# Optimization experiments

Hardware: AMD Instinct MI355X
Metric: run time of the kernel (lower is better)

Reference implementation:

```python
import jax, jax.numpy as jnp
import numpy as np

N_WIRES = 4
DIM = 16  # 2**4 state-vector length; wire 0 = most significant bit


def _ry(state, theta, wire):
    """Apply RY(theta) on `wire`. state: (N,16) real; theta: (N,) or scalar."""
    s = jnp.moveaxis(state.reshape(-1, 2, 2, 2, 2), 1 + wire, 1)
    c = jnp.cos(theta * 0.5)
    sn = jnp.sin(theta * 0.5)
    if jnp.ndim(theta):
        c = c.reshape(-1, 1, 1, 1)
        sn = sn.reshape(-1, 1, 1, 1)
    s0, s1 = s[:, 0], s[:, 1]
    out = jnp.stack([c * s0 - sn * s1, sn * s0 + c * s1], axis=1)
    return jnp.moveaxis(out, 1, 1 + wire).reshape(-1, DIM)


def _cx_perm(control, target):
    idx = np.arange(DIM)
    cbit = (idx >> (N_WIRES - 1 - control)) & 1
    return np.where(cbit == 1, idx ^ (1 << (N_WIRES - 1 - target)), idx)

# Pauli-Z expectation signs per wire: (16, 4)
_Z_SIGNS = np.stack(
    [1.0 - 2.0 * ((np.arange(DIM) >> (N_WIRES - 1 - w)) & 1) for w in range(N_WIRES)],
    axis=1,
).astype(np.float32)
_CX01 = _cx_perm(0, 1); _CX12 = _cx_perm(1, 2); _CX23 = _cx_perm(2, 3)
_CX02 = _cx_perm(0, 2); _CX13 = _cx_perm(1, 3)


def _init_state(n, dtype):
    return jnp.zeros((n, DIM), dtype).at[:, 0].set(1.0)  # |0000>


def _encode(angles):
    """Fresh device + RY(angle_w) on each wire. angles: (N,4) -> state (N,16)."""
    state = _init_state(angles.shape[0], angles.dtype)
    for w in range(N_WIRES):
        state = _ry(state, angles[:, w], w)
    return state


def _measure_z(state):
    return (state * state) @ jnp.asarray(_Z_SIGNS, state.dtype)  # (N,4)


def _quanv_features(angles, rl_params):
    """Encoder + fixed 8-op 'random layer' (5 RY + 3 CX) + MeasureAll(Z)."""
    s = _encode(angles)
    s = _ry(s, rl_params[0], 0)
    s = _ry(s, rl_params[1], 1)
    s = s[:, _CX02]
    s = _ry(s, rl_params[2], 2)
    s = _ry(s, rl_params[3], 3)
    s = s[:, _CX13]
    s = _ry(s, rl_params[4], 0)
    s = s[:, _CX23]
    return _measure_z(s)  # (N,4)


def _attn_raw(angles):
    """Encoder + CX(0,1),CX(1,2),CX(2,3), measure Z on wire 0."""
    s = _encode(angles)
    s = s[:, _CX01]
    s = s[:, _CX12]
    s = s[:, _CX23]
    return _measure_z(s)[:, 0]  # (N,)


def setup_inputs() -> dict:
    key = jax.random.key(0)
    k1, k2, k3 = jax.random.split(key, 3)
    B = 4096
    x = jax.random.uniform(k1, (B, 784), dtype=jnp.float32)
    rl_params = jax.random.normal(k2, (5,), dtype=jnp.float32)
    W = jax.random.normal(k3, (10, 784), dtype=jnp.float32) * 0.03
    b = jnp.zeros((10,), jnp.float32)
    return {"x": x, "rl_params": rl_params, "W": W, "b": b}


def reference(x, rl_params, W, b):
    B = x.shape[0]
    img = x.reshape(B, 28, 28)
    # 2x2 patches in row-major order -> (B*196, 4) with order [tl, tr, bl, br]
    angles = img.reshape(B, 14, 2, 14, 2).transpose(0, 1, 3, 2, 4).reshape(B * 196, 4)
    feats = _quanv_features(angles, rl_params).reshape(B, 196, 4)
    raw = _attn_raw(feats.reshape(B * 196, 4)).reshape(B, 196)
    attn = jax.nn.softmax(raw, axis=1)
    weighted = (feats * attn[:, :, None]).reshape(B, 4 * 14 * 14)
    logits = weighted @ W.T + b
    return jax.nn.log_softmax(logits, axis=-1)
```

## Files before the change

### kernel.cpp

```cpp
#include <hip/hip_runtime.h>

#define NTHREADS 256
#define NPATCH 196


__device__ __forceinline__ float dot4(float4 a, float4 b) {
    return a.x * b.x + a.y * b.y + a.z * b.z + a.w * b.w;
}

__global__ __launch_bounds__(NTHREADS) void quanv_fused(
    const float* __restrict__ x, const float* __restrict__ rl,
    const float* __restrict__ W, const float* __restrict__ bias,
    float* __restrict__ out)
{
    __shared__ float xs[4][784];

    const int lane = threadIdx.x & 63;
    const int wave = threadIdx.x >> 6;
    const int img  = blockIdx.x * 4 + wave;

    const float4* __restrict__ xsrc = reinterpret_cast<const float4*>(x + (size_t)img * 784);
    float4* xd = reinterpret_cast<float4*>(xs[wave]);
    #pragma unroll
    for (int r = 0; r < 3; ++r) xd[lane + 64 * r] = xsrc[lane + 64 * r];
    if (lane < 4) xd[192 + lane] = xsrc[192 + lane];
    __syncthreads();

    float srl2, crl2, srl4, crl4;
    __sincosf(rl[2], &srl2, &crl2);
    __sincosf(rl[4], &srl4, &crl4);
    const float rl0 = rl[0], rl1 = rl[1], rl3v = rl[3];

    const float* xw = xs[wave];
    auto patchf = [&](int p, float& f0, float& f1, float& f2, float& f3) {
        const int pi = p / 14;
        const int base = 56 * pi + 2 * (p - pi * 14);
        const float2 top = *reinterpret_cast<const float2*>(&xw[base]);
        const float2 bot = *reinterpret_cast<const float2*>(&xw[base + 28]);
        float sa, ca; __sincosf(top.x + rl0, &sa, &ca);
        float s2, c2; __sincosf(bot.x, &s2, &c2);
        f1 = __cosf(top.y + rl1);
        const float cd = __cosf(bot.y + rl3v);
        f0 = crl4 * ca - srl4 * sa * s2;
        f2 = crl2 * ca * c2 - srl2 * s2;
        f3 = f1 * cd * f2;
    };

    const int p0 = lane, p1 = lane + 64, p2 = lane + 128, p3 = 192 + lane;
    const bool has4 = (lane < 4);

    float f00, f01, f02, f03; patchf(p0, f00, f01, f02, f03);
    float f10, f11, f12, f13; patchf(p1, f10, f11, f12, f13);
    float f20, f21, f22, f23; patchf(p2, f20, f21, f22, f23);
    float f30, f31, f32, f33; patchf(has4 ? p3 : p0, f30, f31, f32, f33);

    const float e0 = __expf(__cosf(f00));
    const float e1 = __expf(__cosf(f10));
    const float e2 = __expf(__cosf(f20));
    const float e3 = has4 ? __expf(__cosf(f30)) : 0.f;

    float sv = e0 + e1 + e2 + e3;
    #pragma unroll
    for (int off = 32; off > 0; off >>= 1) sv += __shfl_xor(sv, off);
    const float inv = 1.0f / sv;

    const float sc0 = e0 * inv, sc1 = e1 * inv, sc2 = e2 * inv, sc3 = e3 * inv;
    const float4 g0 = make_float4(f00 * sc0, f01 * sc0, f02 * sc0, f03 * sc0);
    const float4 g1 = make_float4(f10 * sc1, f11 * sc1, f12 * sc1, f13 * sc1);
    const float4 g2 = make_float4(f20 * sc2, f21 * sc2, f22 * sc2, f23 * sc2);
    const float4 g3 = make_float4(f30 * sc3, f31 * sc3, f32 * sc3, f33 * sc3);

    const float4* __restrict__ W4 = reinterpret_cast<const float4*>(W);
    float acc[10];
    #pragma unroll
    for (int k = 0; k < 10; ++k) {
        acc[k] = dot4(g0, W4[k * NPATCH + p0])
               + dot4(g1, W4[k * NPATCH + p1])
               + dot4(g2, W4[k * NPATCH + p2]);
    }
    if (has4) {
        #pragma unroll
        for (int k = 0; k < 10; ++k) acc[k] += dot4(g3, W4[k * NPATCH + p3]);
    }

    #pragma unroll
    for (int k = 0; k < 10; ++k) {
        #pragma unroll
        for (int off = 32; off > 0; off >>= 1) acc[k] += __shfl_xor(acc[k], off);
        acc[k] += bias[k];
    }

    float m2 = acc[0];
    #pragma unroll
    for (int k = 1; k < 10; ++k) m2 = fmaxf(m2, acc[k]);
    float ssum = 0.f;
    #pragma unroll
    for (int k = 0; k < 10; ++k) ssum += __expf(acc[k] - m2);
    const float lse = m2 + __logf(ssum);

    if (lane < 10) {
        float myv = acc[0];
        #pragma unroll
        for (int k = 1; k < 10; ++k) myv = (lane == k) ? acc[k] : myv;
        out[(size_t)img * 10 + lane] = myv - lse;
    }
}

extern "C" void kernel_launch(void* const* d_in, const int* in_sizes, int n_in,
                              void* d_out, int out_size, void* d_ws, size_t ws_size,
                              hipStream_t stream) {
    const float* x    = (const float*)d_in[0];
    const float* rl   = (const float*)d_in[1];
    const float* W    = (const float*)d_in[2];
    const float* bias = (const float*)d_in[3];
    float* out = (float*)d_out;
    const int B = in_sizes[0] / 784;
    quanv_fused<<<B / 4, NTHREADS, 0, stream>>>(x, rl, W, bias, out);
}
```

Measured before the change: 13.44 us.

## Split each image across two waves, use DPP reductions, drop LDS staging

```diff
diff --git a/kernel.cpp b/kernel.cpp
--- a/kernel.cpp
+++ b/kernel.cpp
@@ -8,35 +8,50 @@
     return a.x * b.x + a.y * b.y + a.z * b.z + a.w * b.w;
 }
 
-__global__ __launch_bounds__(NTHREADS) void quanv_fused(
+__device__ __forceinline__ float wave_sum63(float x) {
+#define DPP_STEP(ctrl, rmask)                                                   \
+    x += __int_as_float(__builtin_amdgcn_update_dpp(                            \
+        0, __float_as_int(x), (ctrl), (rmask), 0xf, true));
+    DPP_STEP(0x111, 0xf)
+    DPP_STEP(0x112, 0xf)
+    DPP_STEP(0x114, 0xf)
+    DPP_STEP(0x118, 0xf)
+    DPP_STEP(0x142, 0xa)
+    DPP_STEP(0x143, 0xc)
+#undef DPP_STEP
+    return x;
+}
+
+__global__ __launch_bounds__(NTHREADS, 6) void quanv_fused(
     const float* __restrict__ x, const float* __restrict__ rl,
     const float* __restrict__ W, const float* __restrict__ bias,
     float* __restrict__ out)
 {
-    __shared__ float xs[4][784];
+    __shared__ float redw[4];
+    __shared__ float redl[4][10];
 
     const int lane = threadIdx.x & 63;
     const int wave = threadIdx.x >> 6;
-    const int img  = blockIdx.x * 4 + wave;
+    const int il   = wave >> 1;
+    const int half = wave & 1;
+    const int img  = blockIdx.x * 2 + il;
 
-    const float4* __restrict__ xsrc = reinterpret_cast<const float4*>(x + (size_t)img * 784);
-    float4* xd = reinterpret_cast<float4*>(xs[wave]);
-    #pragma unroll
-    for (int r = 0; r < 3; ++r) xd[lane + 64 * r] = xsrc[lane + 64 * r];
-    if (lane < 4) xd[192 + lane] = xsrc[192 + lane];
-    __syncthreads();
+    const float* __restrict__ xb = x + (size_t)img * 784;
 
     float srl2, crl2, srl4, crl4;
     __sincosf(rl[2], &srl2, &crl2);
     __sincosf(rl[4], &srl4, &crl4);
     const float rl0 = rl[0], rl1 = rl[1], rl3v = rl[3];
 
-    const float* xw = xs[wave];
+    const int p0 = half * 98 + lane;
+    const bool has2 = (lane < 34);
+    const int pp1 = has2 ? (p0 + 64) : p0;
+
     auto patchf = [&](int p, float& f0, float& f1, float& f2, float& f3) {
         const int pi = p / 14;
         const int base = 56 * pi + 2 * (p - pi * 14);
-        const float2 top = *reinterpret_cast<const float2*>(&xw[base]);
-        const float2 bot = *reinterpret_cast<const float2*>(&xw[base + 28]);
+        const float2 top = *reinterpret_cast<const float2*>(xb + base);
+        const float2 bot = *reinterpret_cast<const float2*>(xb + base + 28);
         float sa, ca; __sincosf(top.x + rl0, &sa, &ca);
         float s2, c2; __sincosf(bot.x, &s2, &c2);
         f1 = __cosf(top.y + rl1);
@@ -46,63 +61,54 @@
         f3 = f1 * cd * f2;
     };
 
-    const int p0 = lane, p1 = lane + 64, p2 = lane + 128, p3 = 192 + lane;
-    const bool has4 = (lane < 4);
-
-    float f00, f01, f02, f03; patchf(p0, f00, f01, f02, f03);
-    float f10, f11, f12, f13; patchf(p1, f10, f11, f12, f13);
-    float f20, f21, f22, f23; patchf(p2, f20, f21, f22, f23);
-    float f30, f31, f32, f33; patchf(has4 ? p3 : p0, f30, f31, f32, f33);
+    float f00, f01, f02, f03; patchf(p0,  f00, f01, f02, f03);
+    float f10, f11, f12, f13; patchf(pp1, f10, f11, f12, f13);
 
     const float e0 = __expf(__cosf(f00));
-    const float e1 = __expf(__cosf(f10));
-    const float e2 = __expf(__cosf(f20));
-    const float e3 = has4 ? __expf(__cosf(f30)) : 0.f;
+    const float e1 = has2 ? __expf(__cosf(f10)) : 0.f;
 
-    float sv = e0 + e1 + e2 + e3;
-    #pragma unroll
-    for (int off = 32; off > 0; off >>= 1) sv += __shfl_xor(sv, off);
-    const float inv = 1.0f / sv;
+    const float svw = wave_sum63(e0 + e1);
+    if (lane == 63) redw[wave] = svw;
+    __syncthreads();
+    const float inv = 1.0f / (redw[wave & ~1] + redw[wave | 1]);
 
-    const float sc0 = e0 * inv, sc1 = e1 * inv, sc2 = e2 * inv, sc3 = e3 * inv;
+    const float sc0 = e0 * inv, sc1 = e1 * inv;
     const float4 g0 = make_float4(f00 * sc0, f01 * sc0, f02 * sc0, f03 * sc0);
     const float4 g1 = make_float4(f10 * sc1, f11 * sc1, f12 * sc1, f13 * sc1);
-    const float4 g2 = make_float4(f20 * sc2, f21 * sc2, f22 * sc2, f23 * sc2);
-    const float4 g3 = make_float4(f30 * sc3, f31 * sc3, f32 * sc3, f33 * sc3);
 
     const float4* __restrict__ W4 = reinterpret_cast<const float4*>(W);
     float acc[10];
     #pragma unroll
     for (int k = 0; k < 10; ++k) {
-        acc[k] = dot4(g0, W4[k * NPATCH + p0])
-               + dot4(g1, W4[k * NPATCH + p1])
-               + dot4(g2, W4[k * NPATCH + p2]);
-    }
-    if (has4) {
-        #pragma unroll
-        for (int k = 0; k < 10; ++k) acc[k] += dot4(g3, W4[k * NPATCH + p3]);
+        acc[k] = dot4(g0, W4[k * NPATCH + p0]) + dot4(g1, W4[k * NPATCH + pp1]);
     }
 
     #pragma unroll
-    for (int k = 0; k < 10; ++k) {
+    for (int k = 0; k < 10; ++k) acc[k] = wave_sum63(acc[k]);
+    if (lane == 63) {
         #pragma unroll
-        for (int off = 32; off > 0; off >>= 1) acc[k] += __shfl_xor(acc[k], off);
-        acc[k] += bias[k];
+        for (int k = 0; k < 10; ++k) redl[wave][k] = acc[k];
     }
+    __syncthreads();
 
-    float m2 = acc[0];
-    #pragma unroll
-    for (int k = 1; k < 10; ++k) m2 = fmaxf(m2, acc[k]);
-    float ssum = 0.f;
-    #pragma unroll
-    for (int k = 0; k < 10; ++k) ssum += __expf(acc[k] - m2);
-    const float lse = m2 + __logf(ssum);
-
-    if (lane < 10) {
-        float myv = acc[0];
+    if (half == 0) {
+        float lg[10];
         #pragma unroll
-        for (int k = 1; k < 10; ++k) myv = (lane == k) ? acc[k] : myv;
-        out[(size_t)img * 10 + lane] = myv - lse;
+        for (int k = 0; k < 10; ++k)
+            lg[k] = redl[wave][k] + redl[wave + 1][k] + bias[k];
+        float m2 = lg[0];
+        #pragma unroll
+        for (int k = 1; k < 10; ++k) m2 = fmaxf(m2, lg[k]);
+        float ssum = 0.f;
+        #pragma unroll
+        for (int k = 0; k < 10; ++k) ssum += __expf(lg[k] - m2);
+        const float lse = m2 + __logf(ssum);
+        if (lane < 10) {
+            float myv = lg[0];
+            #pragma unroll
+            for (int k = 1; k < 10; ++k) myv = (lane == k) ? lg[k] : myv;
+            out[(size_t)img * 10 + lane] = myv - lse;
+        }
     }
 }
 
@@ -115,5 +121,5 @@
     const float* bias = (const float*)d_in[3];
     float* out = (float*)d_out;
     const int B = in_sizes[0] / 784;
-    quanv_fused<<<B / 4, NTHREADS, 0, stream>>>(x, rl, W, bias, out);
+    quanv_fused<<<B / 2, NTHREADS, 0, stream>>>(x, rl, W, bias, out);
 }
```

Measured after the change: 13.12 us. -2.4%, faster.
